# Kernel optimization log

Hardware: AMD Instinct MI355X
Metric: run time of the kernel (lower is better)

## Reference

```python
import jax, jax.numpy as jnp
import numpy as np

B, T, K, V, D, H = 16, 512, 32, 512, 64, 128


def setup_inputs() -> dict:
    key = jax.random.key(0)
    ks = jax.random.split(key, 10)
    s = lambda k, shape: jax.random.normal(k, shape, jnp.float32) * 0.05
    sequences = jax.random.randint(ks[0], (B, T), 0, V)
    lengths = jax.random.randint(ks[1], (B,), 1, T + 1)
    return dict(
        sequences=sequences,
        lengths=lengths,
        emb=s(ks[2], (V, D)),
        W1=s(ks[3], (D, H)), b1=jnp.zeros((H,), jnp.float32),
        W2=s(ks[4], (H, K * K)), b2=jnp.zeros((K * K,), jnp.float32),
        E1=s(ks[5], (D, H)), e1=jnp.zeros((H,), jnp.float32),
        E2=s(ks[6], (H, K * V)), e2=jnp.zeros((K * V,), jnp.float32),
        init_logits=s(ks[7], (K,)),
    )


def reference(sequences, lengths, emb, W1, b1, W2, b2, E1, e1, E2, e2, init_logits):
    Bc, Tc = sequences.shape
    # shift inputs: start token 0 followed by sequences[:, :-1]
    inputs = jnp.concatenate(
        [jnp.zeros((Bc, 1), sequences.dtype), sequences[:, :-1]], axis=1)
    x = emb[inputs]                                  # (B,T,D)
    # transition net -> (B,T,K,K) row-normalized in log space
    h1 = jax.nn.relu(x @ W1 + b1)
    log_trans = jax.nn.log_softmax((h1 @ W2 + b2).reshape(Bc, Tc, K, K), axis=-1)
    # emission net -> (B,T,K,V), gather observed-token scores
    h2 = jax.nn.relu(x @ E1 + e1)
    log_emit = jax.nn.log_softmax((h2 @ E2 + e2).reshape(Bc, Tc, K, V), axis=-1)
    tgt = jnp.broadcast_to(sequences[:, :, None, None], (Bc, Tc, K, 1))
    emit_scores = jnp.take_along_axis(log_emit, tgt, axis=3)[..., 0]  # (B,T,K)
    init_lp = jax.nn.log_softmax(init_logits)
    alpha0 = init_lp[None, :] + emit_scores[:, 0]    # (B,K)

    def step(alpha, xs):
        lt, es, t = xs                               # (B,K,K),(B,K),()
        new = jax.nn.logsumexp(alpha[:, :, None] + lt, axis=1) + es
        alpha = jnp.where((t < lengths)[:, None], new, alpha)
        return alpha, None

    xs = (jnp.swapaxes(log_trans, 0, 1)[1:],
          jnp.swapaxes(emit_scores, 0, 1)[1:],
          jnp.arange(1, Tc))
    alpha, _ = jax.lax.scan(step, alpha0, xs)
    return -jax.nn.logsumexp(alpha, axis=1)         # (B,) negative log-likelihood
```

## Files before the change

### kernel.cpp

```cpp
#include <hip/hip_runtime.h>
#include <hip/hip_bf16.h>

#define BB 16
#define TT 512
#define KK 32
#define VV 512
#define DD 64
#define HH 128
#define KV (KK*VV)
#define KKK (KK*KK)

#define INV_LN2 1.4426950408889634f
#define LN2 0.6931471805599453f

typedef unsigned short u16;
typedef __attribute__((ext_vector_type(8))) short short8;
typedef __attribute__((ext_vector_type(8))) unsigned short ushort8;
typedef __attribute__((ext_vector_type(16))) float f32x16;
typedef __attribute__((ext_vector_type(4))) unsigned int uint4v;

__device__ __forceinline__ float fexp2(float x) { return __builtin_amdgcn_exp2f(x); }
__device__ __forceinline__ float flog2(float x) { return __builtin_amdgcn_logf(x); }

__device__ __forceinline__ u16 f2bf(float f) {
  unsigned u = __builtin_bit_cast(unsigned, f);
  u += 0x7FFFu + ((u >> 16) & 1u);
  return (u16)(u >> 16);
}
__device__ __forceinline__ float bf2f(u16 v) {
  return __builtin_bit_cast(float, ((unsigned)v) << 16);
}

__device__ __forceinline__ float es_dot(const u16* __restrict__ erow,
                                        const u16* __restrict__ hrow) {
  float a0 = 0.f, a1 = 0.f, a2 = 0.f, a3 = 0.f;
#pragma unroll
  for (int r = 0; r < 8; ++r) {
    short8 ev = ((const short8*)erow)[r];
    short8 hv = ((const short8*)hrow)[r];
    a0 += bf2f((u16)ev[0]) * bf2f((u16)hv[0]);
    a1 += bf2f((u16)ev[1]) * bf2f((u16)hv[1]);
    a2 += bf2f((u16)ev[2]) * bf2f((u16)hv[2]);
    a3 += bf2f((u16)ev[3]) * bf2f((u16)hv[3]);
    a0 += bf2f((u16)ev[4]) * bf2f((u16)hv[4]);
    a1 += bf2f((u16)ev[5]) * bf2f((u16)hv[5]);
    a2 += bf2f((u16)ev[6]) * bf2f((u16)hv[6]);
    a3 += bf2f((u16)ev[7]) * bf2f((u16)hv[7]);
  }
  return (a0 + a1) + (a2 + a3);
}

__device__ __forceinline__ void mul_step(short8 fr0, short8 fr1, int h,
                                         float* D) {
  float e0[8], e1[8];
#pragma unroll
  for (int i2 = 0; i2 < 4; ++i2) {
    float x0 = __shfl_xor(D[i2], 32);
    float y0 = __shfl_xor(D[4 + i2], 32);
    e0[i2] = (h == 0) ? D[i2] : y0;
    e0[4 + i2] = (h == 0) ? x0 : D[4 + i2];
    float x1 = __shfl_xor(D[8 + i2], 32);
    float y1 = __shfl_xor(D[12 + i2], 32);
    e1[i2] = (h == 0) ? D[8 + i2] : y1;
    e1[4 + i2] = (h == 0) ? x1 : D[12 + i2];
  }
  short8 B0, B1;
#pragma unroll
  for (int e = 0; e < 8; ++e) {
    B0[e] = (short)f2bf(e0[e]);
    B1[e] = (short)f2bf(e1[e]);
  }
  f32x16 dn = {};
  dn = __builtin_amdgcn_mfma_f32_32x32x16_bf16(fr0, B0, dn, 0, 0, 0);
  dn = __builtin_amdgcn_mfma_f32_32x32x16_bf16(fr1, B1, dn, 0, 0, 0);
#pragma unroll
  for (int r = 0; r < 16; ++r) D[r] = dn[r];
}

__device__ __forceinline__ void ident_D(int j, int h, float* D) {
#pragma unroll
  for (int r = 0; r < 16; ++r) D[r] = 0.f;
  if (((j >> 2) & 1) == h) D[(j & 3) | ((j >> 3) << 2)] = 1.0f;
}

__global__ __launch_bounds__(256) void k_prep1(
    const float* __restrict__ E2, u16* __restrict__ E2bT,
    u16* __restrict__ E2yT, const float* __restrict__ W2,
    u16* __restrict__ W2T, const float* __restrict__ emb,
    const float* __restrict__ W1, const float* __restrict__ b1,
    const float* __restrict__ E1, const float* __restrict__ e1,
    u16* __restrict__ h1b, u16* __restrict__ h2b) {
  __shared__ float tl[32][65];
  __shared__ float embs[16][64];
  int tid = threadIdx.x;
  int bid = blockIdx.x;

  if (bid < 1088) {
    const float* src;
    u16* dst;
    size_t srcld;
    int c0, h0;
    int isE2 = (bid < 1024);
    if (isE2) {
      c0 = (bid & 255) * 64;
      h0 = (bid >> 8) * 32;
      src = E2;
      dst = E2bT;
      srcld = KV;
    } else {
      int b2i = bid - 1024;
      c0 = (b2i & 15) * 64;
      h0 = (b2i >> 4) * 32;
      src = W2;
      dst = W2T;
      srcld = KKK;
    }
    int r = tid >> 6, c = tid & 63;
#pragma unroll
    for (int rr = 0; rr < 8; ++rr)
      tl[r * 8 + rr][c] = src[(size_t)(h0 + r * 8 + rr) * srcld + c0 + c];
    __syncthreads();
    int cw = tid >> 3, hb = tid & 7;
#pragma unroll
    for (int pass = 0; pass < 2; ++pass) {
      int cc = pass * 32 + cw;
      unsigned lo = (unsigned)f2bf(tl[hb * 4 + 0][cc]) |
                    ((unsigned)f2bf(tl[hb * 4 + 1][cc]) << 16);
      unsigned hi = (unsigned)f2bf(tl[hb * 4 + 2][cc]) |
                    ((unsigned)f2bf(tl[hb * 4 + 3][cc]) << 16);
      uint2 v;
      v.x = lo;
      v.y = hi;
      int col = c0 + cc;
      *(uint2*)(dst + (size_t)col * HH + h0 + hb * 4) = v;
      if (isE2) {
        int k = col >> 9, y = col & 511;
        *(uint2*)(E2yT + ((size_t)y * KK + k) * HH + h0 + hb * 4) = v;
      }
    }
    return;
  }

  int u0 = (bid - 1088) * 16;
#pragma unroll
  for (int it = 0; it < 4; ++it) {
    int idx = it * 256 + tid;
    embs[idx >> 6][idx & 63] = emb[u0 * DD + idx];
  }
  __syncthreads();
  int h = tid & 127, tl2 = tid >> 7;
  float b1v = b1[h], e1v = e1[h];
#pragma unroll
  for (int it = 0; it < 8; ++it) {
    int tok = it * 2 + tl2;
    float a1 = b1v, a2 = e1v;
#pragma unroll 8
    for (int d = 0; d < DD; ++d) {
      float xv = embs[tok][d];
      a1 += xv * W1[d * HH + h];
      a2 += xv * E1[d * HH + h];
    }
    h1b[(u0 + tok) * HH + h] = f2bf(fmaxf(a1, 0.f));
    h2b[(u0 + tok) * HH + h] = f2bf(fmaxf(a2, 0.f));
  }
}

__global__ __launch_bounds__(256) void k_tables(
    const u16* __restrict__ h1b, const u16* __restrict__ W2T,
    const float* __restrict__ b2, float* __restrict__ ltrans,
    const u16* __restrict__ h2b, const u16* __restrict__ E2bT,
    const float* __restrict__ e2, float* __restrict__ lse2_tab) {
  __shared__ float ls[4 * 32];
  int bid = blockIdx.x;
  int tid = threadIdx.x;
  int w = tid >> 6, l = tid & 63;
  int h = l >> 5, j = l & 31;

  if (bid < 512) {
    int k = bid & 31;
    int u0 = (bid >> 5) * 32;

    short8 A[8];
#pragma unroll
    for (int kh = 0; kh < 8; ++kh)
      A[kh] = *(const short8*)(h2b + (u0 + j) * HH + kh * 16 + h * 8);

    float s[16];
#pragma unroll
    for (int r = 0; r < 16; ++r) s[r] = 0.f;

#pragma unroll
    for (int c = 0; c < 4; ++c) {
      int ct = w * 4 + c;
      int col = k * 512 + ct * 32 + j;
      const u16* bp = E2bT + (size_t)col * HH + h * 8;
      f32x16 acc = {};
#pragma unroll
      for (int kh = 0; kh < 8; ++kh) {
        short8 Bf = *(const short8*)(bp + kh * 16);
        acc = __builtin_amdgcn_mfma_f32_32x32x16_bf16(A[kh], Bf, acc, 0, 0, 0);
      }
      float e2v = e2[col] * INV_LN2;
#pragma unroll
      for (int r = 0; r < 16; ++r) s[r] += fexp2(acc[r] * INV_LN2 + e2v);
    }
#pragma unroll
    for (int r = 0; r < 16; ++r) {
#pragma unroll
      for (int d = 1; d < 32; d <<= 1) s[r] += __shfl_xor(s[r], d);
    }
    if (j == 0) {
#pragma unroll
      for (int r = 0; r < 16; ++r) {
        int row = (r & 3) + 8 * (r >> 2) + 4 * h;
        ls[w * 32 + row] = s[r];
      }
    }
    __syncthreads();
    if (tid < 32) {
      float total = ls[tid] + ls[32 + tid] + ls[64 + tid] + ls[96 + tid];
      lse2_tab[(u0 + tid) * KK + k] = flog2(total);
    }
    return;
  }

  int t2 = bid - 512;
  int i = t2 & 31;
  int tt = (t2 >> 5) * 4 + w;
  int u0 = tt * 32;

  f32x16 acc = {};
#pragma unroll
  for (int kh = 0; kh < 8; ++kh) {
    short8 A = *(const short8*)(h1b + (u0 + j) * HH + kh * 16 + h * 8);
    short8 Bf = *(const short8*)(W2T + (i * 32 + j) * HH + kh * 16 + h * 8);
    acc = __builtin_amdgcn_mfma_f32_32x32x16_bf16(A, Bf, acc, 0, 0, 0);
  }
  float b2v = b2[i * 32 + j] * INV_LN2;
  float lgv[16], se[16];
#pragma unroll
  for (int r = 0; r < 16; ++r) {
    lgv[r] = acc[r] * INV_LN2 + b2v;
    se[r] = fexp2(lgv[r]);
  }
#pragma unroll
  for (int r = 0; r < 16; ++r) {
#pragma unroll
    for (int d = 1; d < 32; d <<= 1) se[r] += __shfl_xor(se[r], d);
  }
#pragma unroll
  for (int r = 0; r < 16; ++r) {
    int row = (r & 3) + 8 * (r >> 2) + 4 * h;
    ltrans[(u0 + row) * KKK + j * KK + i] = lgv[r] - flog2(se[r]);
  }
}

__global__ __launch_bounds__(256) void k_matprod(
    const int* __restrict__ seq, const int* __restrict__ lengths,
    const float* __restrict__ ltrans, const u16* __restrict__ h2b,
    const u16* __restrict__ E2yT, const float* __restrict__ e2,
    const float* __restrict__ lse2, u16* __restrict__ C1,
    float* __restrict__ s1) {
  __shared__ float tmp[4][32 * 33];
  int w = threadIdx.x >> 6, l = threadIdx.x & 63;
  int c = blockIdx.x * 4 + w;
  int b = c >> 6, t0 = (c & 63) * 8;
  int j = l & 31, h = l >> 5;
  int len = lengths[b];
  len = (len < 1) ? 1 : ((len > TT) ? TT : len);
  const int* sb = seq + b * TT;
  int tlo = (t0 < 1) ? 1 : t0;
  int thi = (t0 + 8 < len) ? (t0 + 8) : len;

  u16* op = C1 + (size_t)c * 1024 + j * 32 + h * 16;
  if (tlo >= thi) {
    ushort8 w0v, w1v;
#pragma unroll
    for (int e = 0; e < 8; ++e) {
      w0v[e] = ((h * 16 + e) == j) ? (u16)0x3F80 : (u16)0;
      w1v[e] = ((h * 16 + 8 + e) == j) ? (u16)0x3F80 : (u16)0;
    }
    *(ushort8*)op = w0v;
    *(ushort8*)(op + 8) = w1v;
    if (l == 0) s1[c] = 0.f;
    return;
  }

  short8 fr0s[8], fr1s[8];
  float sacc = 0.f;
#pragma unroll
  for (int s = 0; s < 8; ++s) {
    int t = t0 + s;
    if (t >= 1 && t < len) {
      int u = sb[t - 1], y = sb[t];
      float dot = es_dot(E2yT + ((size_t)y * KK + j) * HH + h * 64,
                         h2b + u * HH + h * 64);
      dot += __shfl_xor(dot, 32);
      float esj = (dot + e2[j * VV + y]) * INV_LN2 - lse2[u * KK + j];
      float m = esj;
#pragma unroll
      for (int d = 1; d < 32; d <<= 1) m = fmaxf(m, __shfl_xor(m, d));
      sacc += m;
      const float4* p4 = (const float4*)(ltrans + u * KKK + j * KK + h * 16);
      float4 q0 = p4[0], q1 = p4[1], q2 = p4[2], q3 = p4[3];
      float lgv[16] = {q0.x, q0.y, q0.z, q0.w, q1.x, q1.y, q1.z, q1.w,
                       q2.x, q2.y, q2.z, q2.w, q3.x, q3.y, q3.z, q3.w};
      float off = esj - m;
#pragma unroll
      for (int e = 0; e < 16; ++e) lgv[e] += off;
      unsigned pk[8];
#pragma unroll
      for (int p = 0; p < 8; ++p)
        pk[p] = (unsigned)f2bf(fexp2(lgv[2 * p])) |
                ((unsigned)f2bf(fexp2(lgv[2 * p + 1])) << 16);
      unsigned rcv[4];
#pragma unroll
      for (int p = 0; p < 4; ++p)
        rcv[p] = (unsigned)__shfl_xor((int)(h == 0 ? pk[4 + p] : pk[p]), 32);
      unsigned f0[4], f1[4];
#pragma unroll
      for (int p = 0; p < 4; ++p) {
        f0[p] = h == 0 ? pk[p] : rcv[p];
        f1[p] = h == 0 ? rcv[p] : pk[4 + p];
      }
      fr0s[s] = __builtin_bit_cast(short8, (uint4v){f0[0], f0[1], f0[2], f0[3]});
      fr1s[s] = __builtin_bit_cast(short8, (uint4v){f1[0], f1[1], f1[2], f1[3]});
    } else {
      ushort8 i0, i1;
#pragma unroll
      for (int e = 0; e < 8; ++e) {
        i0[e] = ((h * 8 + e) == j) ? (u16)0x3F80 : (u16)0;
        i1[e] = ((16 + h * 8 + e) == j) ? (u16)0x3F80 : (u16)0;
      }
      fr0s[s] = __builtin_bit_cast(short8, i0);
      fr1s[s] = __builtin_bit_cast(short8, i1);
    }
  }

  float D[16];
  ident_D(j, h, D);
#pragma unroll
  for (int s = 0; s < 8; ++s) mul_step(fr0s[s], fr1s[s], h, D);

  float mx = D[0];
#pragma unroll
  for (int r = 1; r < 16; ++r) mx = fmaxf(mx, D[r]);
#pragma unroll
  for (int d = 1; d < 64; d <<= 1) mx = fmaxf(mx, __shfl_xor(mx, d));
  float inv = 1.0f / mx;
#pragma unroll
  for (int r = 0; r < 16; ++r) {
    int row = (r & 3) + 8 * (r >> 2) + 4 * h;
    tmp[w][row * 33 + j] = D[r] * inv;
  }
  ushort8 w0v, w1v;
#pragma unroll
  for (int e = 0; e < 8; ++e) {
    w0v[e] = f2bf(tmp[w][j * 33 + h * 16 + e]);
    w1v[e] = f2bf(tmp[w][j * 33 + h * 16 + 8 + e]);
  }
  *(ushort8*)op = w0v;
  *(ushort8*)(op + 8) = w1v;
  if (l == 0) s1[c] = flog2(mx) + sacc;
}

__global__ __launch_bounds__(512) void k_final2(
    const u16* __restrict__ C1, const float* __restrict__ s1,
    const int* __restrict__ seq, const u16* __restrict__ h2b,
    const u16* __restrict__ E2yT, const float* __restrict__ e2,
    const float* __restrict__ lse2, const float* __restrict__ init_logits,
    float* __restrict__ out) {
  __shared__ u16 mats[8][1024];
  __shared__ float scs[8];
  int b = blockIdx.x;
  int w = threadIdx.x >> 6, l = threadIdx.x & 63;
  int j = l & 31, h = l >> 5;

  float D[16];
  ident_D(j, h, D);
  const u16* base = C1 + ((size_t)b * 64 + w * 8) * 1024;
#pragma unroll
  for (int s = 0; s < 8; ++s) {
    short8 fr0 = *(const short8*)(base + s * 1024 + j * 32 + h * 8);
    short8 fr1 = *(const short8*)(base + s * 1024 + j * 32 + h * 8 + 16);
    mul_step(fr0, fr1, h, D);
  }
  float mx = D[0];
#pragma unroll
  for (int r = 1; r < 16; ++r) mx = fmaxf(mx, D[r]);
#pragma unroll
  for (int d = 1; d < 64; d <<= 1) mx = fmaxf(mx, __shfl_xor(mx, d));
  float inv = 1.0f / mx;
#pragma unroll
  for (int r = 0; r < 16; ++r) {
    int row = (r & 3) + 8 * (r >> 2) + 4 * h;
    mats[w][row * 32 + j] = f2bf(D[r] * inv);
  }
  float si = (l < 8) ? s1[b * 64 + w * 8 + l] : 0.f;
#pragma unroll
  for (int d = 1; d < 64; d <<= 1) si += __shfl_xor(si, d);
  if (l == 0) scs[w] = flog2(mx) + si;
  __syncthreads();

  if (w == 0) {
    float D2[16];
    ident_D(j, h, D2);
#pragma unroll
    for (int s = 0; s < 8; ++s) {
      short8 fr0 = *(const short8*)(&mats[s][j * 32 + h * 8]);
      short8 fr1 = *(const short8*)(&mats[s][j * 32 + h * 8 + 16]);
      mul_step(fr0, fr1, h, D2);
    }
    int y0 = seq[b * TT];
    float dot = es_dot(E2yT + ((size_t)y0 * KK + j) * HH + h * 64,
                       h2b + h * 64);
    dot += __shfl_xor(dot, 32);
    float esj = (dot + e2[j * VV + y0]) * INV_LN2 - lse2[j];
    float il = init_logits[j] * INV_LN2;
    float m0 = il;
#pragma unroll
    for (int d = 1; d < 32; d <<= 1) m0 = fmaxf(m0, __shfl_xor(m0, d));
    float s0 = fexp2(il - m0);
#pragma unroll
    for (int d = 1; d < 32; d <<= 1) s0 += __shfl_xor(s0, d);
    float lse0 = m0 + flog2(s0);
    float z = il - lse0 + esj;
    float am = z;
#pragma unroll
    for (int d = 1; d < 32; d <<= 1) am = fmaxf(am, __shfl_xor(am, d));
    float a0 = fexp2(z - am);
    float colsum = 0.f;
#pragma unroll
    for (int r = 0; r < 16; ++r) colsum += D2[r];
    float p = a0 * colsum;
#pragma unroll
    for (int d = 1; d < 64; d <<= 1) p += __shfl_xor(p, d);
    float sct = (l < 8) ? scs[l] : 0.f;
#pragma unroll
    for (int d = 1; d < 64; d <<= 1) sct += __shfl_xor(sct, d);
    if (l == 0) out[b] = -LN2 * (flog2(p) + am + sct);
  }
}

extern "C" void kernel_launch(void* const* d_in, const int* in_sizes, int n_in,
                              void* d_out, int out_size, void* d_ws,
                              size_t ws_size, hipStream_t stream) {
  const int* seq = (const int*)d_in[0];
  const int* lengths = (const int*)d_in[1];
  const float* emb = (const float*)d_in[2];
  const float* W1 = (const float*)d_in[3];
  const float* b1 = (const float*)d_in[4];
  const float* W2 = (const float*)d_in[5];
  const float* b2 = (const float*)d_in[6];
  const float* E1 = (const float*)d_in[7];
  const float* e1 = (const float*)d_in[8];
  const float* E2 = (const float*)d_in[9];
  const float* e2 = (const float*)d_in[10];
  const float* init_logits = (const float*)d_in[11];
  float* out = (float*)d_out;

  char* wsb = (char*)d_ws;
  float* ltrans = (float*)(wsb + 0);
  u16* h2b = (u16*)(wsb + 2097152);
  u16* h1b = (u16*)(wsb + 2228224);
  u16* E2bT = (u16*)(wsb + 2359296);
  u16* W2T = (u16*)(wsb + 6553600);
  float* lse2 = (float*)(wsb + 6815744);
  u16* C1 = (u16*)(wsb + 6881280);
  float* s1 = (float*)(wsb + 8978432);
  u16* E2yT = (u16*)(wsb + 8982528);

  k_prep1<<<1120, 256, 0, stream>>>(E2, E2bT, E2yT, W2, W2T, emb, W1, b1, E1,
                                    e1, h1b, h2b);
  k_tables<<<640, 256, 0, stream>>>(h1b, W2T, b2, ltrans, h2b, E2bT, e2, lse2);
  k_matprod<<<256, 256, 0, stream>>>(seq, lengths, ltrans, h2b, E2yT, e2,
                                     lse2, C1, s1);
  k_final2<<<16, 512, 0, stream>>>(C1, s1, seq, h2b, E2yT, e2, lse2,
                                   init_logits, out);
}
```

Baseline: 83.11 us.

## Split each 8-step chunk product across two waves and combine via LDS

Each chunk's eight-step matrix product is now computed by a pair of waves, each doing four steps. The high wave normalizes its partial product, stores it as bf16 in shared memory along with its log-scale, and the low wave multiplies it in with one extra MFMA step. This halves the serial dependent MFMA chain per wave and doubles the waves per block to hide latency. The cost is a block-wide barrier, an extra bf16 rounding of the intermediate product, and one more multiply.

```diff
diff --git a/kernel.cpp b/kernel.cpp
--- a/kernel.cpp
+++ b/kernel.cpp
@@ -255,25 +255,109 @@
   }
 }
 
-__global__ __launch_bounds__(256) void k_matprod(
+#define MSTRIDE 40
+__global__ __launch_bounds__(512) void k_matprod(
     const int* __restrict__ seq, const int* __restrict__ lengths,
     const float* __restrict__ ltrans, const u16* __restrict__ h2b,
     const u16* __restrict__ E2yT, const float* __restrict__ e2,
     const float* __restrict__ lse2, u16* __restrict__ C1,
     float* __restrict__ s1) {
+  __shared__ u16 mats[4][32 * MSTRIDE];
+  __shared__ float scs[8];
   __shared__ float tmp[4][32 * 33];
   int w = threadIdx.x >> 6, l = threadIdx.x & 63;
-  int c = blockIdx.x * 4 + w;
-  int b = c >> 6, t0 = (c & 63) * 8;
+  int pair = w >> 1, hi = w & 1;
+  int c = blockIdx.x * 4 + pair;
+  int b = c >> 6, t0c = (c & 63) * 8;
+  int t0 = t0c + hi * 4;
   int j = l & 31, h = l >> 5;
   int len = lengths[b];
   len = (len < 1) ? 1 : ((len > TT) ? TT : len);
   const int* sb = seq + b * TT;
-  int tlo = (t0 < 1) ? 1 : t0;
-  int thi = (t0 + 8 < len) ? (t0 + 8) : len;
+  int tlo_c = (t0c < 1) ? 1 : t0c;
+  int thi_c = (t0c + 8 < len) ? (t0c + 8) : len;
+  bool fullid = (tlo_c >= thi_c);
+
+  float D[16];
+  ident_D(j, h, D);
+  float sacc = 0.f;
+
+  if (!fullid) {
+    short8 fr0s[4], fr1s[4];
+#pragma unroll
+    for (int s = 0; s < 4; ++s) {
+      int t = t0 + s;
+      if (t >= 1 && t < len) {
+        int u = sb[t - 1], y = sb[t];
+        float dot = es_dot(E2yT + ((size_t)y * KK + j) * HH + h * 64,
+                           h2b + u * HH + h * 64);
+        dot += __shfl_xor(dot, 32);
+        float esj = (dot + e2[j * VV + y]) * INV_LN2 - lse2[u * KK + j];
+        float m = esj;
+#pragma unroll
+        for (int d = 1; d < 32; d <<= 1) m = fmaxf(m, __shfl_xor(m, d));
+        sacc += m;
+        const float4* p4 = (const float4*)(ltrans + u * KKK + j * KK + h * 16);
+        float4 q0 = p4[0], q1 = p4[1], q2 = p4[2], q3 = p4[3];
+        float lgv[16] = {q0.x, q0.y, q0.z, q0.w, q1.x, q1.y, q1.z, q1.w,
+                         q2.x, q2.y, q2.z, q2.w, q3.x, q3.y, q3.z, q3.w};
+        float off = esj - m;
+#pragma unroll
+        for (int e = 0; e < 16; ++e) lgv[e] += off;
+        unsigned pk[8];
+#pragma unroll
+        for (int p = 0; p < 8; ++p)
+          pk[p] = (unsigned)f2bf(fexp2(lgv[2 * p])) |
+                  ((unsigned)f2bf(fexp2(lgv[2 * p + 1])) << 16);
+        unsigned rcv[4];
+#pragma unroll
+        for (int p = 0; p < 4; ++p)
+          rcv[p] = (unsigned)__shfl_xor((int)(h == 0 ? pk[4 + p] : pk[p]), 32);
+        unsigned f0[4], f1[4];
+#pragma unroll
+        for (int p = 0; p < 4; ++p) {
+          f0[p] = h == 0 ? pk[p] : rcv[p];
+          f1[p] = h == 0 ? rcv[p] : pk[4 + p];
+        }
+        fr0s[s] =
+            __builtin_bit_cast(short8, (uint4v){f0[0], f0[1], f0[2], f0[3]});
+        fr1s[s] =
+            __builtin_bit_cast(short8, (uint4v){f1[0], f1[1], f1[2], f1[3]});
+      } else {
+        ushort8 i0, i1;
+#pragma unroll
+        for (int e = 0; e < 8; ++e) {
+          i0[e] = ((h * 8 + e) == j) ? (u16)0x3F80 : (u16)0;
+          i1[e] = ((16 + h * 8 + e) == j) ? (u16)0x3F80 : (u16)0;
+        }
+        fr0s[s] = __builtin_bit_cast(short8, i0);
+        fr1s[s] = __builtin_bit_cast(short8, i1);
+      }
+    }
+
+#pragma unroll
+    for (int s = 0; s < 4; ++s) mul_step(fr0s[s], fr1s[s], h, D);
+
+    if (hi) {
+      float mx = D[0];
+#pragma unroll
+      for (int r = 1; r < 16; ++r) mx = fmaxf(mx, D[r]);
+#pragma unroll
+      for (int d = 1; d < 64; d <<= 1) mx = fmaxf(mx, __shfl_xor(mx, d));
+      float inv = 1.0f / mx;
+#pragma unroll
+      for (int r = 0; r < 16; ++r) {
+        int row = (r & 3) + 8 * (r >> 2) + 4 * h;
+        mats[pair][row * MSTRIDE + j] = f2bf(D[r] * inv);
+      }
+      if (l == 0) scs[w] = flog2(mx) + sacc;
+    }
+  }
+  __syncthreads();
+  if (hi) return;
 
   u16* op = C1 + (size_t)c * 1024 + j * 32 + h * 16;
-  if (tlo >= thi) {
+  if (fullid) {
     ushort8 w0v, w1v;
 #pragma unroll
     for (int e = 0; e < 8; ++e) {
@@ -286,61 +370,11 @@
     return;
   }
 
-  short8 fr0s[8], fr1s[8];
-  float sacc = 0.f;
-#pragma unroll
-  for (int s = 0; s < 8; ++s) {
-    int t = t0 + s;
-    if (t >= 1 && t < len) {
-      int u = sb[t - 1], y = sb[t];
-      float dot = es_dot(E2yT + ((size_t)y * KK + j) * HH + h * 64,
-                         h2b + u * HH + h * 64);
-      dot += __shfl_xor(dot, 32);
-      float esj = (dot + e2[j * VV + y]) * INV_LN2 - lse2[u * KK + j];
-      float m = esj;
-#pragma unroll
-      for (int d = 1; d < 32; d <<= 1) m = fmaxf(m, __shfl_xor(m, d));
-      sacc += m;
-      const float4* p4 = (const float4*)(ltrans + u * KKK + j * KK + h * 16);
-      float4 q0 = p4[0], q1 = p4[1], q2 = p4[2], q3 = p4[3];
-      float lgv[16] = {q0.x, q0.y, q0.z, q0.w, q1.x, q1.y, q1.z, q1.w,
-                       q2.x, q2.y, q2.z, q2.w, q3.x, q3.y, q3.z, q3.w};
-      float off = esj - m;
-#pragma unroll
-      for (int e = 0; e < 16; ++e) lgv[e] += off;
-      unsigned pk[8];
-#pragma unroll
-      for (int p = 0; p < 8; ++p)
-        pk[p] = (unsigned)f2bf(fexp2(lgv[2 * p])) |
-                ((unsigned)f2bf(fexp2(lgv[2 * p + 1])) << 16);
-      unsigned rcv[4];
-#pragma unroll
-      for (int p = 0; p < 4; ++p)
-        rcv[p] = (unsigned)__shfl_xor((int)(h == 0 ? pk[4 + p] : pk[p]), 32);
-      unsigned f0[4], f1[4];
-#pragma unroll
-      for (int p = 0; p < 4; ++p) {
-        f0[p] = h == 0 ? pk[p] : rcv[p];
-        f1[p] = h == 0 ? rcv[p] : pk[4 + p];
-      }
-      fr0s[s] = __builtin_bit_cast(short8, (uint4v){f0[0], f0[1], f0[2], f0[3]});
-      fr1s[s] = __builtin_bit_cast(short8, (uint4v){f1[0], f1[1], f1[2], f1[3]});
-    } else {
-      ushort8 i0, i1;
-#pragma unroll
-      for (int e = 0; e < 8; ++e) {
-        i0[e] = ((h * 8 + e) == j) ? (u16)0x3F80 : (u16)0;
-        i1[e] = ((16 + h * 8 + e) == j) ? (u16)0x3F80 : (u16)0;
-      }
-      fr0s[s] = __builtin_bit_cast(short8, i0);
-      fr1s[s] = __builtin_bit_cast(short8, i1);
-    }
-  }
-
-  float D[16];
-  ident_D(j, h, D);
-#pragma unroll
-  for (int s = 0; s < 8; ++s) mul_step(fr0s[s], fr1s[s], h, D);
+  {
+    short8 fr0 = *(const short8*)(&mats[pair][j * MSTRIDE + h * 8]);
+    short8 fr1 = *(const short8*)(&mats[pair][j * MSTRIDE + h * 8 + 16]);
+    mul_step(fr0, fr1, h, D);
+  }
 
   float mx = D[0];
 #pragma unroll
@@ -351,17 +385,17 @@
 #pragma unroll
   for (int r = 0; r < 16; ++r) {
     int row = (r & 3) + 8 * (r >> 2) + 4 * h;
-    tmp[w][row * 33 + j] = D[r] * inv;
+    tmp[pair][row * 33 + j] = D[r] * inv;
   }
   ushort8 w0v, w1v;
 #pragma unroll
   for (int e = 0; e < 8; ++e) {
-    w0v[e] = f2bf(tmp[w][j * 33 + h * 16 + e]);
-    w1v[e] = f2bf(tmp[w][j * 33 + h * 16 + 8 + e]);
+    w0v[e] = f2bf(tmp[pair][j * 33 + h * 16 + e]);
+    w1v[e] = f2bf(tmp[pair][j * 33 + h * 16 + 8 + e]);
   }
   *(ushort8*)op = w0v;
   *(ushort8*)(op + 8) = w1v;
-  if (l == 0) s1[c] = flog2(mx) + sacc;
+  if (l == 0) s1[c] = flog2(mx) + sacc + scs[w + 1];
 }
 
 __global__ __launch_bounds__(512) void k_final2(
@@ -473,7 +507,7 @@
   k_prep1<<<1120, 256, 0, stream>>>(E2, E2bT, E2yT, W2, W2T, emb, W1, b1, E1,
                                     e1, h1b, h2b);
   k_tables<<<640, 256, 0, stream>>>(h1b, W2T, b2, ltrans, h2b, E2bT, e2, lse2);
-  k_matprod<<<256, 256, 0, stream>>>(seq, lengths, ltrans, h2b, E2yT, e2,
+  k_matprod<<<256, 512, 0, stream>>>(seq, lengths, ltrans, h2b, E2yT, e2,
                                      lse2, C1, s1);
   k_final2<<<16, 512, 0, stream>>>(C1, s1, seq, h2b, E2yT, e2, lse2,
                                    init_logits, out);
```

After: 81.60 us. About the same (-1.8%).
